# Optimization experiments

Hardware: AMD Instinct MI355X
Metric: run time of the kernel (lower is better)

The kernel has to match this reference:

```python
import jax, jax.numpy as jnp
import numpy as np

HEADS = 16
DIM_HEAD = 64
BLOCK = 16
SEQ_LEN = 2048
NUM_BLOCKS = SEQ_LEN // BLOCK  # 128
NUM_RANDOM_BLOCKS = 32
LOCAL_WINDOW = 4
GLOBAL_BLOCKS = [0]


def make_layout():
    # Deterministic stand-in for DeepSpeed VariableSparsityConfig.make_layout
    # (local windows of 4 blocks + random blocks + global block columns/rows,
    #  then tril for unidirectional attention).
    rng = np.random.RandomState(0)
    nb = NUM_BLOCKS
    layout = np.zeros((nb, nb), dtype=bool)
    for w in range(0, nb, LOCAL_WINDOW):
        layout[w:w + LOCAL_WINDOW, w:w + LOCAL_WINDOW] = True
    rnd = rng.randint(0, nb, size=(nb, NUM_RANDOM_BLOCKS))
    layout[np.arange(nb)[:, None], rnd] = True
    for g in GLOBAL_BLOCKS:
        layout[:, g] = True
        layout[g, :] = True
    layout = np.tril(layout)  # unidirectional
    return jnp.asarray(layout)


def setup_inputs() -> dict:
    key = jax.random.key(0)
    k1, k2, k3 = jax.random.split(key, 3)
    dim = 1024
    inner = HEADS * DIM_HEAD  # 1024
    x = jax.random.normal(k1, (2, SEQ_LEN, dim), dtype=jnp.float32)
    w_qkv = jax.random.normal(k2, (dim, 3 * inner), dtype=jnp.float32) * 0.02
    w_out = jax.random.normal(k3, (inner, dim), dtype=jnp.float32) * 0.02
    b_out = jnp.zeros((dim,), dtype=jnp.float32)
    layout = make_layout()  # [128, 128] bool
    return {"x": x, "w_qkv": w_qkv, "w_out": w_out, "b_out": b_out, "layout": layout}


def reference(x, w_qkv, w_out, b_out, layout):
    b, n, _ = x.shape
    scale = DIM_HEAD ** -0.5
    qkv = x @ w_qkv  # [b, n, 3*h*d]
    q, k, v = jnp.split(qkv, 3, axis=-1)
    split_heads = lambda t: t.reshape(b, n, HEADS, DIM_HEAD).transpose(0, 2, 1, 3)
    q, k, v = split_heads(q), split_heads(k), split_heads(v)  # [b, h, n, d]

    scores = jnp.einsum('bhid,bhjd->bhij', q, k) * scale  # [b, h, n, n]
    neg = -jnp.finfo(scores.dtype).max
    # additive causal attn_mask (value = -finfo.max / 2, attn_mask_mode='add')
    causal = jnp.triu(jnp.ones((n, n), dtype=bool), 1)
    scores = scores + jnp.where(causal, neg / 2, jnp.zeros((), scores.dtype))
    # block-sparse layout: entries outside allowed blocks are fully masked
    allowed = jnp.repeat(jnp.repeat(layout, BLOCK, axis=0), BLOCK, axis=1)  # [n, n]
    scores = jnp.where(allowed, scores, neg)
    attn = jax.nn.softmax(scores, axis=-1)
    out = jnp.einsum('bhij,bhjd->bhid', attn, v)  # [b, h, n, d]
    out = out.transpose(0, 2, 1, 3).reshape(b, n, HEADS * DIM_HEAD)
    return out @ w_out + b_out
```

## Files before the change

kernel.cpp:

```cpp
#include <hip/hip_runtime.h>
#include <cstdint>
#include <cstddef>


typedef short bf8 __attribute__((ext_vector_type(8)));
typedef float f32x4 __attribute__((ext_vector_type(4)));
typedef unsigned short u16;
typedef unsigned int u32;

#define MFMA_BF16(a, b, c) __builtin_amdgcn_mfma_f32_16x16x32_bf16((a), (b), (c), 0, 0, 0)

constexpr int SEQ = 2048;
constexpr int NH = 16;
constexpr int DHD = 64;
constexpr int NBLK = 128;
constexpr int DIM = 1024;

__device__ __forceinline__ u16 f2bf(float f) {
  unsigned u = __float_as_uint(f);
  return (u16)((u + 0x7fffu + ((u >> 16) & 1u)) >> 16);
}
__device__ __forceinline__ u32 pack2bf(float a, float b) {
  return (u32)f2bf(a) | ((u32)f2bf(b) << 16);
}
__device__ __forceinline__ void gload_lds16(const u16* g, u16* l) {
  auto gp = (const __attribute__((address_space(1))) u16*)(g);
  auto lp = (__attribute__((address_space(3))) u16*)(l);
  __builtin_amdgcn_global_load_lds(gp, lp, 16, 0, 0);
}

__global__ __launch_bounds__(256) void prep(
    const float* __restrict__ x, u16* __restrict__ xbf,
    const float* __restrict__ wqkv, u16* __restrict__ wqkvT,
    const float* __restrict__ wout, u16* __restrict__ woutT,
    const unsigned char* __restrict__ lay,
    int* __restrict__ cnt, int* __restrict__ cols) {
  __shared__ u16 tile[64][72];
  int bid = blockIdx.x;
  int t = threadIdx.x;

  if (bid < 2048) {
    int idx = (bid * 256 + t) * 8;
    float4 a = *(const float4*)(x + idx);
    float4 b = *(const float4*)(x + idx + 4);
    *(ushort4*)(xbf + idx)     = make_ushort4(f2bf(a.x), f2bf(a.y), f2bf(a.z), f2bf(a.w));
    *(ushort4*)(xbf + idx + 4) = make_ushort4(f2bf(b.x), f2bf(b.y), f2bf(b.z), f2bf(b.w));
    return;
  }
  bid -= 2048;
  if (bid < 768 + 256) {
    const float* in; u16* out; int C, bx, by;
    if (bid < 768) { in = wqkv; out = wqkvT; C = 3072; bx = bid % 48; by = bid / 48; }
    else { int r = bid - 768; in = wout; out = woutT; C = 1024; bx = r % 16; by = r / 16; }
    const int R = 1024;
    int c0 = bx * 64, r0 = by * 64;
    int rr = t >> 4, cc = (t & 15) * 4;
    #pragma unroll
    for (int p = 0; p < 64; p += 16) {
      float4 v = *(const float4*)(in + (size_t)(r0 + rr + p) * C + c0 + cc);
      tile[rr + p][cc + 0] = f2bf(v.x);
      tile[rr + p][cc + 1] = f2bf(v.y);
      tile[rr + p][cc + 2] = f2bf(v.z);
      tile[rr + p][cc + 3] = f2bf(v.w);
    }
    __syncthreads();
    int oc = t >> 3, orr = (t & 7) * 8;
    #pragma unroll
    for (int p = 0; p < 64; p += 32) {
      u16 tmp[8];
      #pragma unroll
      for (int qy = 0; qy < 8; qy++) tmp[qy] = tile[orr + qy][oc + p];
      u16* dst = out + (size_t)(c0 + oc + p) * R + r0 + orr;
      *(ushort4*)(dst)     = make_ushort4(tmp[0], tmp[1], tmp[2], tmp[3]);
      *(ushort4*)(dst + 4) = make_ushort4(tmp[4], tmp[5], tmp[6], tmp[7]);
    }
    return;
  }
  bid -= 1024;
  int wave = t >> 6, lane = t & 63;
  int i = bid * 4 + wave;
  const uint4* l4 = (const uint4*)lay;
  u32 acc = 0;
  #pragma unroll
  for (int it = 0; it < 16; it++) {
    uint4 v = l4[it * 64 + lane];
    acc |= ((v.x | v.y | v.z | v.w) & 0xFFFFFF00u);
  }
  bool as_int32 = (__ballot(acc != 0) == 0ULL);
  const int* li = (const int*)lay;
  int j0 = lane, j1 = lane + 64;
  bool p0 = (j0 <= i) && (as_int32 ? (li[i * 128 + j0] != 0) : (lay[i * 128 + j0] != 0));
  bool p1 = (j1 <= i) && (as_int32 ? (li[i * 128 + j1] != 0) : (lay[i * 128 + j1] != 0));
  unsigned long long m0 = __ballot(p0), m1 = __ballot(p1);
  unsigned long long lt = (1ULL << lane) - 1ULL;
  int base0 = __popcll(m0);
  if (p0) cols[i * 128 + __popcll(m0 & lt)] = j0;
  if (p1) cols[i * 128 + base0 + __popcll(m1 & lt)] = j1;
  if (lane == 0) cnt[i] = base0 + __popcll(m1);
}

__global__ __launch_bounds__(256) void gemm_qkv(
    const u16* __restrict__ A, const u16* __restrict__ Bt,
    u16* __restrict__ oq, u16* __restrict__ okk, u16* __restrict__ ov) {
  __shared__ u16 smem[16896];
  u16* bA0 = smem;
  u16* bB0 = smem + 4096;
  u16* bA1 = smem + 8192;
  u16* bB1 = smem + 12288;
  const int K = 1024;
  int tid = threadIdx.x, lane = tid & 63, wave = tid >> 6;
  int quad = lane >> 4, l16 = lane & 15;
  int wr = wave >> 1, wc = wave & 1;
  int d = blockIdx.x;
  int xcd = d & 7, rest = d >> 3;
  int bm = xcd + (rest & 3) * 8;
  int bn = rest >> 2;
  int bm0 = bm * 128, bn0 = bn * 128;

  f32x4 acc[4][4];
  #pragma unroll
  for (int i = 0; i < 4; i++)
    #pragma unroll
    for (int j = 0; j < 4; j++) acc[i][j] = (f32x4){0.f, 0.f, 0.f, 0.f};

  int srow = lane >> 2;
  int schunk = ((lane & 3) ^ (srow & 3)) * 8;
  int phys = (quad ^ (l16 & 3)) * 8;

  auto stage = [&](u16* dA, u16* dB, int k0) {
    #pragma unroll
    for (int r = 0; r < 2; r++) {
      int row = wave * 32 + r * 16;
      gload_lds16(A  + (size_t)(bm0 + row + srow) * K + k0 + schunk, dA + row * 32);
      gload_lds16(Bt + (size_t)(bn0 + row + srow) * K + k0 + schunk, dB + row * 32);
    }
  };
  auto compute = [&](const u16* cA, const u16* cB) {
    bf8 af[4], bfr[4];
    #pragma unroll
    for (int i = 0; i < 4; i++)
      af[i] = *(const bf8*)(cA + (wr * 64 + i * 16 + l16) * 32 + phys);
    #pragma unroll
    for (int j = 0; j < 4; j++)
      bfr[j] = *(const bf8*)(cB + (wc * 64 + j * 16 + l16) * 32 + phys);
    #pragma unroll
    for (int i = 0; i < 4; i++)
      #pragma unroll
      for (int j = 0; j < 4; j++)
        acc[i][j] = MFMA_BF16(af[i], bfr[j], acc[i][j]);
  };

  stage(bA0, bB0, 0);
  for (int k0 = 0; k0 < K; k0 += 64) {
    __syncthreads();
    if (k0 + 32 < K) stage(bA1, bB1, k0 + 32);
    compute(bA0, bB0);
    __syncthreads();
    if (k0 + 64 < K) stage(bA0, bB0, k0 + 64);
    compute(bA1, bB1);
  }

  int which = bn0 >> 10;
  if (which == 2) {
    #pragma unroll
    for (int j = 0; j < 4; j++) {
      int c = bn0 + wc * 64 + j * 16 + l16;
      int h = (c & 1023) >> 6, dd = c & 63;
      #pragma unroll
      for (int i = 0; i < 4; i++) {
        int r0 = bm0 + wr * 64 + i * 16;
        int b = r0 >> 11, nn0 = r0 & 2047, jb = nn0 >> 4;
        u16* dst = ov + ((size_t)((b * NH + h) * NBLK + jb) * DHD + dd) * 16 + quad * 4;
        *(ushort4*)dst = make_ushort4(f2bf(acc[i][j][0]), f2bf(acc[i][j][1]),
                                      f2bf(acc[i][j][2]), f2bf(acc[i][j][3]));
      }
    }
  } else {
    u16* dstbase = (which == 0) ? oq : okk;
    __syncthreads();
    #pragma unroll
    for (int j = 0; j < 4; j++) {
      int col = wc * 64 + j * 16 + l16;
      #pragma unroll
      for (int i = 0; i < 4; i++) {
        int row = wr * 64 + i * 16 + quad * 4;
        *(uint2*)&smem[col * 132 + row] =
            make_uint2(pack2bf(acc[i][j][0], acc[i][j][1]),
                       pack2bf(acc[i][j][2], acc[i][j][3]));
      }
    }
    __syncthreads();
    int r = tid >> 1, half = tid & 1;
    int rglob = bm0 + r;
    int b = rglob >> 11, nn = rglob & 2047;
    int h = ((bn0 & 1023) >> 6) + half;
    #pragma unroll
    for (int j = 0; j < 4; j++) {
      union { u16 t[16]; uint4 q[2]; } tv;
      #pragma unroll
      for (int dd = 0; dd < 16; dd++)
        tv.t[dd] = smem[(half * 64 + j * 16 + dd) * 132 + r];
      u16* dst = dstbase + ((size_t)(b * NH + h) * SEQ + nn) * DHD + j * 16;
      *(uint4*)(dst) = tv.q[0];
      *(uint4*)(dst + 8) = tv.q[1];
    }
  }
}

__global__ __launch_bounds__(256) void gemm_out(
    const u16* __restrict__ A, const u16* __restrict__ Bt,
    float* __restrict__ of, const float* __restrict__ bias) {
  __shared__ u16 smem[12288];
  u16* bA0 = smem;
  u16* bB0 = smem + 4096;
  u16* bA1 = smem + 6144;
  u16* bB1 = smem + 10240;
  const int K = 1024, N = 1024;
  int tid = threadIdx.x, lane = tid & 63, wave = tid >> 6;
  int quad = lane >> 4, l16 = lane & 15;
  int wr = wave >> 1, wc = wave & 1;
  int d = blockIdx.x;
  int xcd = d & 7, slot = d >> 3;
  int bm = xcd * 4 + (slot & 3);
  int bn = slot >> 2;
  int bm0 = bm * 128, bn0 = bn * 64;

  f32x4 acc[4][2];
  #pragma unroll
  for (int i = 0; i < 4; i++)
    #pragma unroll
    for (int j = 0; j < 2; j++) acc[i][j] = (f32x4){0.f, 0.f, 0.f, 0.f};

  int srow = lane >> 2;
  int schunk = ((lane & 3) ^ (srow & 3)) * 8;
  int phys = (quad ^ (l16 & 3)) * 8;

  auto stage = [&](u16* dA, u16* dB, int k0) {
    #pragma unroll
    for (int r = 0; r < 2; r++) {
      int row = wave * 32 + r * 16;
      gload_lds16(A + (size_t)(bm0 + row + srow) * K + k0 + schunk, dA + row * 32);
    }
    int brow = wave * 16;
    gload_lds16(Bt + (size_t)(bn0 + brow + srow) * K + k0 + schunk, dB + brow * 32);
  };
  auto compute = [&](const u16* cA, const u16* cB) {
    bf8 af[4], bfr[2];
    #pragma unroll
    for (int i = 0; i < 4; i++)
      af[i] = *(const bf8*)(cA + (wr * 64 + i * 16 + l16) * 32 + phys);
    #pragma unroll
    for (int j = 0; j < 2; j++)
      bfr[j] = *(const bf8*)(cB + (wc * 32 + j * 16 + l16) * 32 + phys);
    #pragma unroll
    for (int i = 0; i < 4; i++)
      #pragma unroll
      for (int j = 0; j < 2; j++)
        acc[i][j] = MFMA_BF16(af[i], bfr[j], acc[i][j]);
  };

  stage(bA0, bB0, 0);
  for (int k0 = 0; k0 < K; k0 += 64) {
    __syncthreads();
    if (k0 + 32 < K) stage(bA1, bB1, k0 + 32);
    compute(bA0, bB0);
    __syncthreads();
    if (k0 + 64 < K) stage(bA0, bB0, k0 + 64);
    compute(bA1, bB1);
  }

  #pragma unroll
  for (int j = 0; j < 2; j++) {
    int c = bn0 + wc * 32 + j * 16 + l16;
    float bv = bias[c];
    #pragma unroll
    for (int i = 0; i < 4; i++) {
      int rbase = bm0 + wr * 64 + i * 16 + quad * 4;
      #pragma unroll
      for (int ii = 0; ii < 4; ii++)
        of[(size_t)(rbase + ii) * N + c] = acc[i][j][ii] + bv;
    }
  }
}

__global__ __launch_bounds__(256) void attn_sparse(
    const u16* __restrict__ q, const u16* __restrict__ k, const u16* __restrict__ vblk,
    const int* __restrict__ cnt, const int* __restrict__ cols,
    u16* __restrict__ aout) {
  __shared__ u32 pbuf[4][320];
  int wave = threadIdx.x >> 6, lane = threadIdx.x & 63;
  int quad = lane >> 4, l16 = lane & 15;
  int blk = blockIdx.x;
  int xcd = blk & 7, rest = blk >> 3;
  int bh = xcd * 4 + (rest & 3);
  int strip = rest >> 2;
  int qb = 127 - (strip * 4 + wave);
  const float scale = 0.125f;
  u32* pbw = pbuf[wave];

  const u16* qp = q + ((size_t)bh * SEQ + qb * 16) * DHD + l16 * DHD + quad * 8;
  bf8 qa0 = *(const bf8*)(qp);
  bf8 qa1 = *(const bf8*)(qp + 32);

  float l_i = 0.f;
  f32x4 o[4];
  #pragma unroll
  for (int t = 0; t < 4; t++) o[t] = (f32x4){0.f, 0.f, 0.f, 0.f};

  int count = cnt[qb];
  const int* mc = cols + qb * NBLK;

  bf8 bufA[8], bufB[8];
  int ja0 = 0, ja1 = 0, jb0b = 0, jb1b = 0;
  bool hvA = false, hvB = false;

  auto ldpair = [&](int p, bf8* kv, int& o0, int& o1, bool& ohv) {
    o0 = mc[p];
    ohv = (p + 1 < count);
    o1 = ohv ? mc[p + 1] : o0;
    const u16* kp0 = k + ((size_t)bh * SEQ + o0 * 16) * DHD + l16 * DHD + quad * 8;
    kv[0] = *(const bf8*)(kp0); kv[1] = *(const bf8*)(kp0 + 32);
    const u16* kp1 = k + ((size_t)bh * SEQ + o1 * 16) * DHD + l16 * DHD + quad * 8;
    kv[2] = *(const bf8*)(kp1); kv[3] = *(const bf8*)(kp1 + 32);
    int jq = (quad < 2) ? o0 : o1;
    const u16* vp = vblk + (size_t)(bh * NBLK + jq) * 1024 + l16 * 16 + (quad & 1) * 8;
    kv[4] = *(const bf8*)(vp);
    kv[5] = *(const bf8*)(vp + 256);
    kv[6] = *(const bf8*)(vp + 512);
    kv[7] = *(const bf8*)(vp + 768);
  };

  ldpair(0, bufA, ja0, ja1, hvA);
  if (2 < count) ldpair(2, bufB, jb0b, jb1b, hvB);

  for (int p = 0; p < count; p += 2) {
    f32x4 S0 = (f32x4){0.f, 0.f, 0.f, 0.f};
    S0 = MFMA_BF16(bufA[0], qa0, S0);
    S0 = MFMA_BF16(bufA[1], qa1, S0);
    f32x4 S1 = (f32x4){0.f, 0.f, 0.f, 0.f};
    S1 = MFMA_BF16(bufA[2], qa0, S1);
    S1 = MFMA_BF16(bufA[3], qa1, S1);

    float e0[4], e1[4];
    #pragma unroll
    for (int r = 0; r < 4; r++) {
      int kl = quad * 4 + r;
      float s0 = S0[r] * scale;
      if (ja0 == qb && kl > l16) s0 = -1e38f;
      float s1 = hvA ? S1[r] * scale : -1e38f;
      if (hvA && ja1 == qb && kl > l16) s1 = -1e38f;
      e0[r] = __expf(s0);
      e1[r] = __expf(s1);
      l_i += e0[r] + e1[r];
    }

    *(uint2*)(&pbw[l16 * 20 + quad * 2]) =
        make_uint2(pack2bf(e0[0], e0[1]), pack2bf(e0[2], e0[3]));
    *(uint2*)(&pbw[l16 * 20 + 8 + quad * 2]) =
        make_uint2(pack2bf(e1[0], e1[1]), pack2bf(e1[2], e1[3]));
    union { uint4 w; bf8 v; } pf;
    pf.w = *(const uint4*)(&pbw[l16 * 20 + quad * 4]);

    o[0] = MFMA_BF16(bufA[4], pf.v, o[0]);
    o[1] = MFMA_BF16(bufA[5], pf.v, o[1]);
    o[2] = MFMA_BF16(bufA[6], pf.v, o[2]);
    o[3] = MFMA_BF16(bufA[7], pf.v, o[3]);

    #pragma unroll
    for (int z = 0; z < 8; z++) bufA[z] = bufB[z];
    ja0 = jb0b; ja1 = jb1b; hvA = hvB;
    if (p + 4 < count) ldpair(p + 4, bufB, jb0b, jb1b, hvB);
  }

  float l = l_i;
  l += __shfl_xor(l, 16);
  l += __shfl_xor(l, 32);
  float inv = 1.0f / l;
  int b = bh >> 4, h = bh & 15;
  int n = qb * 16 + l16;
  u16* dst = aout + ((size_t)b * SEQ + n) * DIM + h * DHD;
  #pragma unroll
  for (int t = 0; t < 4; t++) {
    ushort4 st = make_ushort4(f2bf(o[t][0] * inv), f2bf(o[t][1] * inv),
                              f2bf(o[t][2] * inv), f2bf(o[t][3] * inv));
    *(ushort4*)(dst + t * 16 + quad * 4) = st;
  }
}

extern "C" void kernel_launch(void* const* d_in, const int* in_sizes, int n_in,
                              void* d_out, int out_size, void* d_ws, size_t ws_size,
                              hipStream_t stream) {
  const float* x      = (const float*)d_in[0];
  const float* w_qkv  = (const float*)d_in[1];
  const float* w_out  = (const float*)d_in[2];
  const float* b_out  = (const float*)d_in[3];
  const unsigned char* layout = (const unsigned char*)d_in[4];
  float* out = (float*)d_out;

  char* ws = (char*)d_ws;
  u16* xbf   = (u16*)(ws);
  u16* wqkvT = (u16*)(ws + (8u  << 20));
  u16* woutT = (u16*)(ws + (14u << 20) + (512u << 10));
  u16* qB    = (u16*)(ws + (17u << 20));
  u16* kB    = (u16*)(ws + (25u << 20));
  u16* vblk  = (u16*)(ws + (33u << 20));
  u16* aout  = (u16*)(ws + (41u << 20));
  int* cnt   = (int*)(ws + (49u << 20));
  int* cols  = (int*)(ws + (49u << 20) + 4096);

  prep<<<3104, 256, 0, stream>>>(x, xbf, w_qkv, wqkvT, w_out, woutT,
                                 layout, cnt, cols);
  gemm_qkv<<<768, 256, 0, stream>>>(xbf, wqkvT, qB, kB, vblk);
  attn_sparse<<<1024, 256, 0, stream>>>(qB, kB, vblk, cnt, cols, aout);
  gemm_out<<<512, 256, 0, stream>>>(aout, woutT, out, b_out);
}
```

Before: 165.2 us.

## Use hardware bf16 pack conversion, fold softmax scale into Q, add MFMA priority

Replaces the software round-to-nearest bf16 conversion with the v_cvt_pk_bf16_f32 instruction everywhere. The attention scale times log2(e) is folded into Q at the QKV projection epilogue, so the attention loop can use exp2f without a per-score multiply. s_setprio is raised around the MFMA groups in the attention loop to favour matrix issue. The Q values are rounded to bf16 after scaling, which slightly changes precision, and the max-free softmax keeps its existing overflow risk.

```diff
diff --git a/kernel.cpp b/kernel.cpp
--- a/kernel.cpp
+++ b/kernel.cpp
@@ -16,12 +16,10 @@
 constexpr int NBLK = 128;
 constexpr int DIM = 1024;
 
-__device__ __forceinline__ u16 f2bf(float f) {
-  unsigned u = __float_as_uint(f);
-  return (u16)((u + 0x7fffu + ((u >> 16) & 1u)) >> 16);
-}
 __device__ __forceinline__ u32 pack2bf(float a, float b) {
-  return (u32)f2bf(a) | ((u32)f2bf(b) << 16);
+  u32 r;
+  asm("v_cvt_pk_bf16_f32 %0, %1, %2" : "=v"(r) : "v"(a), "v"(b));
+  return r;
 }
 __device__ __forceinline__ void gload_lds16(const u16* g, u16* l) {
   auto gp = (const __attribute__((address_space(1))) u16*)(g);
@@ -43,8 +41,8 @@
     int idx = (bid * 256 + t) * 8;
     float4 a = *(const float4*)(x + idx);
     float4 b = *(const float4*)(x + idx + 4);
-    *(ushort4*)(xbf + idx)     = make_ushort4(f2bf(a.x), f2bf(a.y), f2bf(a.z), f2bf(a.w));
-    *(ushort4*)(xbf + idx + 4) = make_ushort4(f2bf(b.x), f2bf(b.y), f2bf(b.z), f2bf(b.w));
+    *(uint4*)(xbf + idx) = make_uint4(pack2bf(a.x, a.y), pack2bf(a.z, a.w),
+                                      pack2bf(b.x, b.y), pack2bf(b.z, b.w));
     return;
   }
   bid -= 2048;
@@ -58,10 +56,8 @@
     #pragma unroll
     for (int p = 0; p < 64; p += 16) {
       float4 v = *(const float4*)(in + (size_t)(r0 + rr + p) * C + c0 + cc);
-      tile[rr + p][cc + 0] = f2bf(v.x);
-      tile[rr + p][cc + 1] = f2bf(v.y);
-      tile[rr + p][cc + 2] = f2bf(v.z);
-      tile[rr + p][cc + 3] = f2bf(v.w);
+      *(u32*)&tile[rr + p][cc + 0] = pack2bf(v.x, v.y);
+      *(u32*)&tile[rr + p][cc + 2] = pack2bf(v.z, v.w);
     }
     __syncthreads();
     int oc = t >> 3, orr = (t & 7) * 8;
@@ -171,12 +167,13 @@
         int r0 = bm0 + wr * 64 + i * 16;
         int b = r0 >> 11, nn0 = r0 & 2047, jb = nn0 >> 4;
         u16* dst = ov + ((size_t)((b * NH + h) * NBLK + jb) * DHD + dd) * 16 + quad * 4;
-        *(ushort4*)dst = make_ushort4(f2bf(acc[i][j][0]), f2bf(acc[i][j][1]),
-                                      f2bf(acc[i][j][2]), f2bf(acc[i][j][3]));
+        *(uint2*)dst = make_uint2(pack2bf(acc[i][j][0], acc[i][j][1]),
+                                  pack2bf(acc[i][j][2], acc[i][j][3]));
       }
     }
   } else {
     u16* dstbase = (which == 0) ? oq : okk;
+    float m = (which == 0) ? 0.18033688f : 1.0f;
     __syncthreads();
     #pragma unroll
     for (int j = 0; j < 4; j++) {
@@ -185,8 +182,8 @@
       for (int i = 0; i < 4; i++) {
         int row = wr * 64 + i * 16 + quad * 4;
         *(uint2*)&smem[col * 132 + row] =
-            make_uint2(pack2bf(acc[i][j][0], acc[i][j][1]),
-                       pack2bf(acc[i][j][2], acc[i][j][3]));
+            make_uint2(pack2bf(acc[i][j][0] * m, acc[i][j][1] * m),
+                       pack2bf(acc[i][j][2] * m, acc[i][j][3] * m));
       }
     }
     __syncthreads();
@@ -295,7 +292,6 @@
   int bh = xcd * 4 + (rest & 3);
   int strip = rest >> 2;
   int qb = 127 - (strip * 4 + wave);
-  const float scale = 0.125f;
   u32* pbw = pbuf[wave];
 
   const u16* qp = q + ((size_t)bh * SEQ + qb * 16) * DHD + l16 * DHD + quad * 8;
@@ -334,23 +330,25 @@
   if (2 < count) ldpair(2, bufB, jb0b, jb1b, hvB);
 
   for (int p = 0; p < count; p += 2) {
+    __builtin_amdgcn_s_setprio(1);
     f32x4 S0 = (f32x4){0.f, 0.f, 0.f, 0.f};
     S0 = MFMA_BF16(bufA[0], qa0, S0);
     S0 = MFMA_BF16(bufA[1], qa1, S0);
     f32x4 S1 = (f32x4){0.f, 0.f, 0.f, 0.f};
     S1 = MFMA_BF16(bufA[2], qa0, S1);
     S1 = MFMA_BF16(bufA[3], qa1, S1);
+    __builtin_amdgcn_s_setprio(0);
 
     float e0[4], e1[4];
     #pragma unroll
     for (int r = 0; r < 4; r++) {
       int kl = quad * 4 + r;
-      float s0 = S0[r] * scale;
+      float s0 = S0[r];
       if (ja0 == qb && kl > l16) s0 = -1e38f;
-      float s1 = hvA ? S1[r] * scale : -1e38f;
+      float s1 = hvA ? S1[r] : -1e38f;
       if (hvA && ja1 == qb && kl > l16) s1 = -1e38f;
-      e0[r] = __expf(s0);
-      e1[r] = __expf(s1);
+      e0[r] = exp2f(s0);
+      e1[r] = exp2f(s1);
       l_i += e0[r] + e1[r];
     }
 
@@ -361,10 +359,12 @@
     union { uint4 w; bf8 v; } pf;
     pf.w = *(const uint4*)(&pbw[l16 * 20 + quad * 4]);
 
+    __builtin_amdgcn_s_setprio(1);
     o[0] = MFMA_BF16(bufA[4], pf.v, o[0]);
     o[1] = MFMA_BF16(bufA[5], pf.v, o[1]);
     o[2] = MFMA_BF16(bufA[6], pf.v, o[2]);
     o[3] = MFMA_BF16(bufA[7], pf.v, o[3]);
+    __builtin_amdgcn_s_setprio(0);
 
     #pragma unroll
     for (int z = 0; z < 8; z++) bufA[z] = bufB[z];
@@ -381,9 +381,9 @@
   u16* dst = aout + ((size_t)b * SEQ + n) * DIM + h * DHD;
   #pragma unroll
   for (int t = 0; t < 4; t++) {
-    ushort4 st = make_ushort4(f2bf(o[t][0] * inv), f2bf(o[t][1] * inv),
-                              f2bf(o[t][2] * inv), f2bf(o[t][3] * inv));
-    *(ushort4*)(dst + t * 16 + quad * 4) = st;
+    *(uint2*)(dst + t * 16 + quad * 4) =
+        make_uint2(pack2bf(o[t][0] * inv, o[t][1] * inv),
+                   pack2bf(o[t][2] * inv, o[t][3] * inv));
   }
 }
 
```

New measurement: 165.2 us. Within noise of the previous version (-0.0%).
